# Kernel tuning notes

Measured on AMD Instinct MI355X. Metric: run time of the kernel, lower is better.

The kernel has to match this reference:

```python
import jax, jax.numpy as jnp
import numpy as np
import math

NUM_HEADS = 16
EMBED = 1024
B, S = 128, 512


def setup_inputs() -> dict:
    key = jax.random.key(0)
    ks = jax.random.split(key, 9)
    scale = 1.0 / math.sqrt(EMBED)
    return {
        "queries": jax.random.normal(ks[0], (B, S, EMBED), dtype=jnp.float32),
        "keys": jax.random.normal(ks[1], (B, S, EMBED), dtype=jnp.float32),
        "values": jax.random.normal(ks[2], (B, S, EMBED), dtype=jnp.float32),
        "Wq": jax.random.normal(ks[3], (EMBED, EMBED), dtype=jnp.float32) * scale,
        "bq": jax.random.normal(ks[4], (EMBED,), dtype=jnp.float32) * scale,
        "Wk": jax.random.normal(ks[5], (EMBED, EMBED), dtype=jnp.float32) * scale,
        "bk": jax.random.normal(ks[6], (EMBED,), dtype=jnp.float32) * scale,
        "Wv": jax.random.normal(ks[7], (EMBED, EMBED), dtype=jnp.float32) * scale,
        "bv": jax.random.normal(ks[8], (EMBED,), dtype=jnp.float32) * scale,
    }


def reference(queries, keys, values, Wq, bq, Wk, bk, Wv, bv):
    H = NUM_HEADS
    E = queries.shape[-1]
    d = E // H
    # torch nn.Linear: y = x @ W.T + b
    q = queries @ Wq.T + bq  # [B, S, E]
    k = keys @ Wk.T + bk
    v = values @ Wv.T + bv
    n_q = q.shape[1]
    n_k = k.shape[1]
    n_v = v.shape[1]
    # Faithful to the original: reshape with seq-len as the LEADING dim,
    # which reinterprets the (B, S, E) buffer as (S, B, H, d).
    q = q.reshape(n_q, -1, H, d)  # [S, B, H, d]
    k = k.reshape(n_k, -1, H, d)
    # attention over the second (batch-like) axis; scores: [S, H, B, B]
    scores = jnp.einsum('nqhd,nkhd->nhqk', q, k) / math.sqrt(d)
    attn = jax.nn.softmax(scores, axis=-1)
    v = v.reshape(n_v, -1, H, d)  # [S, B, H, d]
    out = jnp.einsum('nhql,nlhd->nqhd', attn, v)  # [S, B, H, d]
    n_a = out.shape[0]
    return out.reshape(-1, n_a, H * d)  # [B, S, E]
```

## Files before the change

kernel.cpp:

```cpp
#include <hip/hip_runtime.h>
#include <hip/hip_bf16.h>

typedef unsigned short u16;
typedef __attribute__((ext_vector_type(8))) short bf16x8;
typedef __attribute__((ext_vector_type(4))) float f32x4;
typedef __attribute__((ext_vector_type(4))) float vfloat4;
typedef __attribute__((ext_vector_type(4))) unsigned short ushort4v;
typedef __attribute__((ext_vector_type(8))) unsigned short ushort8v;

#define DEV __device__ __forceinline__
#define AS1 __attribute__((address_space(1)))
#define AS3 __attribute__((address_space(3)))

#define BARRIER()  __builtin_amdgcn_s_barrier()
#define LGKM0()    asm volatile("s_waitcnt lgkmcnt(0)" ::: "memory")
#define VMCNT0()   asm volatile("s_waitcnt vmcnt(0)" ::: "memory")
#define VMCNT4()   asm volatile("s_waitcnt vmcnt(4)" ::: "memory")
#define SCHED0()   __builtin_amdgcn_sched_barrier(0)

DEV u16 f2bf(float f) {
    union { float f; unsigned u; } v; v.f = f;
    unsigned r = v.u + 0x7FFFu + ((v.u >> 16) & 1u);
    return (u16)(r >> 16);
}

DEV void gload_lds16(const void* g, void* l) {
    __builtin_amdgcn_global_load_lds((const AS1 unsigned int*)g,
                                     (AS3 unsigned int*)l, 16, 0, 0);
}

static constexpr int KDIM = 1024;
static constexpr int NROW = 65536;

__global__ __launch_bounds__(256)
void cvt_f32_bf16(const float* __restrict__ src, u16* __restrict__ dst, unsigned n8)
{
    unsigned stride = gridDim.x * blockDim.x;
    for (unsigned i = blockIdx.x * blockDim.x + threadIdx.x; i < n8; i += stride) {
        size_t base = (size_t)i * 8;
        vfloat4 a = *(const vfloat4*)(src + base);
        vfloat4 b = *(const vfloat4*)(src + base + 4);
        ushort8v o;
#pragma unroll
        for (int j = 0; j < 4; ++j) { o[j] = f2bf(a[j]); o[j + 4] = f2bf(b[j]); }
        *(ushort8v*)(dst + base) = o;
    }
}

__global__ __launch_bounds__(512)
__attribute__((amdgpu_waves_per_eu(1, 2)))
void proj_gemm_8ph(const u16* __restrict__ X, const u16* __restrict__ W,
                   const float* __restrict__ bias, u16* __restrict__ Y)
{
    __shared__ __align__(16) u16 As[2][256 * 64];
    __shared__ __align__(16) u16 Bs[2][256 * 64];

    int bx = blockIdx.x;
    int wg = (bx & 7) * 128 + (bx >> 3);
    int bm = wg >> 2;
    int bn = wg & 3;

    int tid  = threadIdx.x;
    int lane = tid & 63;
    int wid  = tid >> 6;
    int wm   = wid >> 2;
    int wn   = wid & 3;
    int l15  = lane & 15;
    int l4   = lane >> 4;

    const u16* Xp = X + (size_t)bm * 256 * KDIM;
    const u16* Wp = W + (size_t)bn * 256 * KDIM;

    int srow_in = tid >> 3;
    int scol16  = (tid & 7) ^ (srow_in & 7);

    f32x4 acc[8][4] = {};

#define STAGE(lds, gbase, slot, h, kt)                                           \
    {                                                                            \
        const u16* src_ = (gbase) + (size_t)((h) * 128 + srow_in) * KDIM         \
                          + (kt) * 64 + scol16 * 8;                              \
        gload_lds16(src_, &lds[slot][((h) * 128 + wid * 8) * 64]);               \
        gload_lds16(src_ + (size_t)64 * KDIM,                                    \
                    &lds[slot][((h) * 128 + 64 + wid * 8) * 64]);                \
    }

#define READ_AF(slot, mh)                                                        \
    {                                                                            \
        _Pragma("unroll")                                                        \
        for (int mi = 0; mi < 4; ++mi) {                                         \
            int row = wm * 128 + (mh) * 64 + mi * 16 + l15;                      \
            unsigned o0 = (unsigned)(row * 128 + l4 * 16) ^ (unsigned)((row & 7) << 4); \
            af[mi][0] = *(const bf16x8*)((const char*)As[slot] + o0);            \
            af[mi][1] = *(const bf16x8*)((const char*)As[slot] + (o0 ^ 64u));    \
        }                                                                        \
    }

#define READ_BF(dst, slot, nh)                                                   \
    {                                                                            \
        _Pragma("unroll")                                                        \
        for (int ni = 0; ni < 2; ++ni) {                                         \
            int row = wn * 64 + (nh) * 32 + ni * 16 + l15;                       \
            unsigned o0 = (unsigned)(row * 128 + l4 * 16) ^ (unsigned)((row & 7) << 4); \
            dst[ni][0] = *(const bf16x8*)((const char*)Bs[slot] + o0);           \
            dst[ni][1] = *(const bf16x8*)((const char*)Bs[slot] + (o0 ^ 64u));   \
        }                                                                        \
    }

#define MFMA_Q(mlo, bb, nlo)                                                     \
    __builtin_amdgcn_s_setprio(1);                                               \
    _Pragma("unroll")                                                            \
    for (int kk = 0; kk < 2; ++kk) {                                             \
        _Pragma("unroll")                                                        \
        for (int mi = 0; mi < 4; ++mi) {                                         \
            _Pragma("unroll")                                                    \
            for (int ni = 0; ni < 2; ++ni)                                       \
                acc[(mlo) + mi][(nlo) + ni] = __builtin_amdgcn_mfma_f32_16x16x32_bf16( \
                    af[mi][kk], bb[ni][kk], acc[(mlo) + mi][(nlo) + ni], 0, 0, 0); \
        }                                                                        \
    }                                                                            \
    __builtin_amdgcn_s_setprio(0);

    STAGE(As, Xp, 0, 0, 0);
    STAGE(As, Xp, 0, 1, 0);
    STAGE(Bs, Wp, 0, 0, 0);
    STAGE(Bs, Wp, 0, 1, 0);
    STAGE(As, Xp, 1, 0, 1);
    STAGE(As, Xp, 1, 1, 1);
    STAGE(Bs, Wp, 1, 0, 1);
    STAGE(Bs, Wp, 1, 1, 1);
    VMCNT0();
    BARRIER();

    for (int it = 0; it < 8; ++it) {
        int c12 = 2 * it + 1;
        int c36 = (2 * it + 2 < 16) ? 2 * it + 2 : 15;
        int c78 = (2 * it + 3 < 16) ? 2 * it + 3 : 15;
        bf16x8 af[4][2], b0[2][2], b1[2][2];

        READ_AF(0, 0); READ_BF(b0, 0, 0);
        STAGE(As, Xp, 1, 0, c12);
        BARRIER(); LGKM0(); SCHED0();
        MFMA_Q(0, b0, 0);
        BARRIER();

        READ_BF(b1, 0, 1);
        STAGE(As, Xp, 1, 1, c12);
        BARRIER(); LGKM0(); SCHED0();
        MFMA_Q(0, b1, 2);
        BARRIER();

        READ_AF(0, 1);
        STAGE(Bs, Wp, 0, 0, c36);
        BARRIER(); LGKM0(); SCHED0();
        MFMA_Q(4, b1, 2);
        BARRIER();

        STAGE(Bs, Wp, 0, 1, c36);
        VMCNT4(); BARRIER(); SCHED0();
        MFMA_Q(4, b0, 0);
        BARRIER();

        READ_AF(1, 0); READ_BF(b0, 1, 0);
        STAGE(As, Xp, 0, 0, c36);
        BARRIER(); LGKM0(); SCHED0();
        MFMA_Q(0, b0, 0);
        BARRIER();

        READ_BF(b1, 1, 1);
        STAGE(As, Xp, 0, 1, c36);
        BARRIER(); LGKM0(); SCHED0();
        MFMA_Q(0, b1, 2);
        BARRIER();

        READ_AF(1, 1);
        STAGE(Bs, Wp, 1, 0, c78);
        BARRIER(); LGKM0(); SCHED0();
        MFMA_Q(4, b1, 2);
        BARRIER();

        STAGE(Bs, Wp, 1, 1, c78);
        VMCNT4(); BARRIER(); SCHED0();
        MFMA_Q(4, b0, 0);
        BARRIER();
    }
    VMCNT0();
    BARRIER();

    u16* Cs = &As[0][0];
#pragma unroll
    for (int p = 0; p < 2; ++p) {
        if (wm == p) {
#pragma unroll
            for (int ni = 0; ni < 4; ++ni) {
                float bv = bias[bn * 256 + wn * 64 + ni * 16 + l15];
#pragma unroll
                for (int mi = 0; mi < 8; ++mi) {
                    int lr0 = mi * 16 + l4 * 4;
                    int c   = wn * 64 + ni * 16 + l15;
#pragma unroll
                    for (int r = 0; r < 4; ++r)
                        Cs[(lr0 + r) * 256 + c] = f2bf(acc[mi][ni][r] + bv);
                }
            }
        }
        __syncthreads();
#pragma unroll
        for (int i = 0; i < 8; ++i) {
            int idx = tid + i * 512;
            int row = idx >> 5;
            int c16 = idx & 31;
            ushort8v v = *(const ushort8v*)&Cs[row * 256 + c16 * 8];
            *(ushort8v*)&Y[(size_t)(bm * 256 + p * 128 + row) * KDIM
                           + bn * 256 + c16 * 8] = v;
        }
        __syncthreads();
    }
#undef STAGE
#undef READ_AF
#undef READ_BF
#undef MFMA_Q
}

__global__ __launch_bounds__(256)
void proj_gemm(const float* __restrict__ X, const float* __restrict__ W,
               const float* __restrict__ bias, u16* __restrict__ Y)
{
    __shared__ u16 As[128 * 64];
    __shared__ u16 Bs[128 * 64];

    int bx = blockIdx.x;
    int wg = (bx & 7) * 512 + (bx >> 3);
    int bm = wg >> 3;
    int bn = wg & 7;

    int tid  = threadIdx.x;
    int lane = tid & 63;
    int wid  = tid >> 6;
    int wrow = (wid >> 1) * 64;
    int wcol = (wid & 1) * 64;
    int l15 = lane & 15;
    int l4  = lane >> 4;

    int srow = tid >> 4;
    int scol = (tid & 15) * 4;

    const float* Xp = X + (size_t)bm * 128 * KDIM;
    const float* Wp = W + (size_t)bn * 128 * KDIM;

    f32x4 acc[4][4] = {};

    for (int k0 = 0; k0 < KDIM; k0 += 64) {
        __syncthreads();
#pragma unroll
        for (int r = 0; r < 8; ++r) {
            int row = r * 16 + srow;
            vfloat4 a = *(const vfloat4*)(Xp + (size_t)row * KDIM + k0 + scol);
            vfloat4 b = *(const vfloat4*)(Wp + (size_t)row * KDIM + k0 + scol);
            ushort4v ap, bp;
#pragma unroll
            for (int j = 0; j < 4; ++j) { ap[j] = f2bf(a[j]); bp[j] = f2bf(b[j]); }
            unsigned off = (unsigned)(row * 128 + scol * 2) ^ (unsigned)((row & 7) << 4);
            *(ushort4v*)((char*)As + off) = ap;
            *(ushort4v*)((char*)Bs + off) = bp;
        }
        __syncthreads();
#pragma unroll
        for (int kk = 0; kk < 2; ++kk) {
            bf16x8 af[4], bfr[4];
#pragma unroll
            for (int mi = 0; mi < 4; ++mi) {
                int row = wrow + mi * 16 + l15;
                unsigned off = (unsigned)(row * 128 + kk * 64 + l4 * 16) ^ (unsigned)((row & 7) << 4);
                af[mi] = *(const bf16x8*)((char*)As + off);
            }
#pragma unroll
            for (int ni = 0; ni < 4; ++ni) {
                int row = wcol + ni * 16 + l15;
                unsigned off = (unsigned)(row * 128 + kk * 64 + l4 * 16) ^ (unsigned)((row & 7) << 4);
                bfr[ni] = *(const bf16x8*)((char*)Bs + off);
            }
#pragma unroll
            for (int mi = 0; mi < 4; ++mi)
#pragma unroll
                for (int ni = 0; ni < 4; ++ni)
                    acc[mi][ni] = __builtin_amdgcn_mfma_f32_16x16x32_bf16(
                        af[mi], bfr[ni], acc[mi][ni], 0, 0, 0);
        }
    }

#pragma unroll
    for (int ni = 0; ni < 4; ++ni) {
        int col = bn * 128 + wcol + ni * 16 + l15;
        float bv = bias[col];
#pragma unroll
        for (int mi = 0; mi < 4; ++mi) {
            int row0 = bm * 128 + wrow + mi * 16 + l4 * 4;
#pragma unroll
            for (int r = 0; r < 4; ++r)
                Y[(size_t)(row0 + r) * KDIM + col] = f2bf(acc[mi][ni][r] + bv);
        }
    }
}

__global__ __launch_bounds__(256)
void attn_kernel(const u16* __restrict__ Qg, const u16* __restrict__ Kg,
                 const u16* __restrict__ Vg, float* __restrict__ Out)
{
    __shared__ u16 Qs[128 * 64];
    __shared__ u16 KVs[64 * 136];
    __shared__ u16 Ps[128 * 136];

    int g = blockIdx.x >> 4;
    int h = blockIdx.x & 15;

    int tid  = threadIdx.x;
    int lane = tid & 63;
    int wid  = tid >> 6;
    int l15 = lane & 15, l4 = lane >> 4;
    int qbase = wid * 32;

    size_t rowbase = (size_t)g * 128 * 1024 + (size_t)h * 64;

    {
        int r  = tid >> 1;
        int c0 = (tid & 1) * 32;
        const u16* qsrc = Qg + rowbase + (size_t)r * 1024 + c0;
        const u16* ksrc = Kg + rowbase + (size_t)r * 1024 + c0;
#pragma unroll
        for (int i = 0; i < 4; ++i) {
            ushort8v qv = *(const ushort8v*)(qsrc + i * 8);
            ushort8v kv = *(const ushort8v*)(ksrc + i * 8);
            unsigned off = (unsigned)(r * 128 + (c0 + i * 8) * 2) ^ (unsigned)((r & 7) << 4);
            *(ushort8v*)((char*)Qs + off) = qv;
            *(ushort8v*)((char*)KVs + off) = kv;
        }
    }
    __syncthreads();

    f32x4 st[8][2] = {};
#pragma unroll
    for (int kk = 0; kk < 2; ++kk) {
        bf16x8 kf[8];
#pragma unroll
        for (int mi = 0; mi < 8; ++mi) {
            int row = mi * 16 + l15;
            unsigned off = (unsigned)(row * 128 + kk * 64 + l4 * 16) ^ (unsigned)((row & 7) << 4);
            kf[mi] = *(const bf16x8*)((char*)KVs + off);
        }
#pragma unroll
        for (int qi = 0; qi < 2; ++qi) {
            int row = qbase + qi * 16 + l15;
            unsigned off = (unsigned)(row * 128 + kk * 64 + l4 * 16) ^ (unsigned)((row & 7) << 4);
            bf16x8 qf = *(const bf16x8*)((char*)Qs + off);
#pragma unroll
            for (int mi = 0; mi < 8; ++mi)
                st[mi][qi] = __builtin_amdgcn_mfma_f32_16x16x32_bf16(kf[mi], qf, st[mi][qi], 0, 0, 0);
        }
    }
    __syncthreads();

    {
        int r  = tid >> 1;
        int c0 = (tid & 1) * 32;
        const u16* vsrc = Vg + rowbase + (size_t)r * 1024 + c0;
#pragma unroll
        for (int i = 0; i < 4; ++i) {
            ushort8v vv = *(const ushort8v*)(vsrc + i * 8);
#pragma unroll
            for (int e = 0; e < 8; ++e)
                KVs[(c0 + i * 8 + e) * 136 + r] = vv[e];
        }
    }

    const float cexp = 0.125f * 1.44269504088896f;
#pragma unroll
    for (int qi = 0; qi < 2; ++qi) {
        float m = -3.0e38f;
#pragma unroll
        for (int mi = 0; mi < 8; ++mi)
#pragma unroll
            for (int r = 0; r < 4; ++r) m = fmaxf(m, st[mi][qi][r]);
        m = fmaxf(m, __shfl_xor(m, 16));
        m = fmaxf(m, __shfl_xor(m, 32));
        float s = 0.f;
#pragma unroll
        for (int mi = 0; mi < 8; ++mi)
#pragma unroll
            for (int r = 0; r < 4; ++r) {
                float p = exp2f((st[mi][qi][r] - m) * cexp);
                st[mi][qi][r] = p;
                s += p;
            }
        s += __shfl_xor(s, 16);
        s += __shfl_xor(s, 32);
        float inv = 1.0f / s;
        int q = qbase + qi * 16 + l15;
#pragma unroll
        for (int mi = 0; mi < 8; ++mi) {
            ushort4v pp;
#pragma unroll
            for (int r = 0; r < 4; ++r) pp[r] = f2bf(st[mi][qi][r] * inv);
            *(ushort4v*)((char*)Ps + (unsigned)(q * 272 + mi * 32 + l4 * 8)) = pp;
        }
    }
    __syncthreads();

    f32x4 o[2][4] = {};
#pragma unroll
    for (int kk = 0; kk < 4; ++kk) {
        bf16x8 pa[2];
#pragma unroll
        for (int mf = 0; mf < 2; ++mf) {
            int q = qbase + mf * 16 + l15;
            pa[mf] = *(const bf16x8*)((char*)Ps + (unsigned)(q * 272 + kk * 64 + l4 * 16));
        }
#pragma unroll
        for (int nf = 0; nf < 4; ++nf) {
            int d = nf * 16 + l15;
            bf16x8 vb = *(const bf16x8*)((char*)KVs + (unsigned)(d * 272 + kk * 64 + l4 * 16));
#pragma unroll
            for (int mf = 0; mf < 2; ++mf)
                o[mf][nf] = __builtin_amdgcn_mfma_f32_16x16x32_bf16(pa[mf], vb, o[mf][nf], 0, 0, 0);
        }
    }

#pragma unroll
    for (int mf = 0; mf < 2; ++mf)
#pragma unroll
        for (int nf = 0; nf < 4; ++nf) {
            int d  = nf * 16 + l15;
            int q0 = qbase + mf * 16 + l4 * 4;
#pragma unroll
            for (int r = 0; r < 4; ++r)
                Out[(size_t)(g * 128 + q0 + r) * 1024 + h * 64 + d] = o[mf][nf][r];
        }
}

extern "C" void kernel_launch(void* const* d_in, const int* in_sizes, int n_in,
                              void* d_out, int out_size, void* d_ws, size_t ws_size,
                              hipStream_t stream)
{
    const float* Xq = (const float*)d_in[0];
    const float* Xk = (const float*)d_in[1];
    const float* Xv = (const float*)d_in[2];
    const float* Wq = (const float*)d_in[3];
    const float* bq = (const float*)d_in[4];
    const float* Wk = (const float*)d_in[5];
    const float* bk = (const float*)d_in[6];
    const float* Wv = (const float*)d_in[7];
    const float* bv = (const float*)d_in[8];

    const size_t NE = (size_t)NROW * KDIM;
    const size_t WE = (size_t)KDIM * KDIM;

    u16* Qw = (u16*)d_ws;
    u16* Kw = Qw + NE;
    u16* Vw = Kw + NE;

    size_t need = NE * 2 * 3 + NE * 2 + WE * 2 * 3;

    if (ws_size >= need) {
        u16* Xb  = Vw + NE;
        u16* Wb0 = Xb + NE;
        u16* Wb1 = Wb0 + WE;
        u16* Wb2 = Wb1 + WE;

        cvt_f32_bf16<<<dim3(512),  dim3(256), 0, stream>>>(Wq, Wb0, (unsigned)(WE / 8));
        cvt_f32_bf16<<<dim3(512),  dim3(256), 0, stream>>>(Wk, Wb1, (unsigned)(WE / 8));
        cvt_f32_bf16<<<dim3(512),  dim3(256), 0, stream>>>(Wv, Wb2, (unsigned)(WE / 8));

        cvt_f32_bf16<<<dim3(2048), dim3(256), 0, stream>>>(Xq, Xb, (unsigned)(NE / 8));
        proj_gemm_8ph<<<dim3(1024), dim3(512), 0, stream>>>(Xb, Wb0, bq, Qw);
        cvt_f32_bf16<<<dim3(2048), dim3(256), 0, stream>>>(Xk, Xb, (unsigned)(NE / 8));
        proj_gemm_8ph<<<dim3(1024), dim3(512), 0, stream>>>(Xb, Wb1, bk, Kw);
        cvt_f32_bf16<<<dim3(2048), dim3(256), 0, stream>>>(Xv, Xb, (unsigned)(NE / 8));
        proj_gemm_8ph<<<dim3(1024), dim3(512), 0, stream>>>(Xb, Wb2, bv, Vw);
    } else {
        proj_gemm<<<dim3(4096), dim3(256), 0, stream>>>(Xq, Wq, bq, Qw);
        proj_gemm<<<dim3(4096), dim3(256), 0, stream>>>(Xk, Wk, bk, Kw);
        proj_gemm<<<dim3(4096), dim3(256), 0, stream>>>(Xv, Wv, bv, Vw);
    }

    attn_kernel<<<dim3(512 * 16), dim3(256), 0, stream>>>(Qw, Kw, Vw, (float*)d_out);
}
```

Measured before the change: 846.8 us.

## Merge GEMM main-loop phases into four and XOR-swizzle epilogue staging buffer

Restructures the main GEMM loop from eight barrier-separated phases into four, issuing both B-fragment reads and both staging loads per phase and running two MFMA quads per phase. This halves the number of barriers and waits per iteration. It also applies an XOR swizzle to the shared-memory epilogue buffer to reduce LDS bank conflicts on both the scattered writes and the vectorized reads. The risks are higher register pressure and less fine-grained interleaving of global loads with compute.

```diff
diff --git a/kernel.cpp b/kernel.cpp
--- a/kernel.cpp
+++ b/kernel.cpp
@@ -138,50 +138,28 @@
         int c78 = (2 * it + 3 < 16) ? 2 * it + 3 : 15;
         bf16x8 af[4][2], b0[2][2], b1[2][2];
 
-        READ_AF(0, 0); READ_BF(b0, 0, 0);
-        STAGE(As, Xp, 1, 0, c12);
+        READ_AF(0, 0); READ_BF(b0, 0, 0); READ_BF(b1, 0, 1);
+        STAGE(As, Xp, 1, 0, c12); STAGE(As, Xp, 1, 1, c12);
         BARRIER(); LGKM0(); SCHED0();
-        MFMA_Q(0, b0, 0);
+        MFMA_Q(0, b0, 0); MFMA_Q(0, b1, 2);
         BARRIER();
 
-        READ_BF(b1, 0, 1);
-        STAGE(As, Xp, 1, 1, c12);
+        READ_AF(0, 1);
+        STAGE(Bs, Wp, 0, 0, c36); STAGE(Bs, Wp, 0, 1, c36);
+        VMCNT4(); BARRIER(); LGKM0(); SCHED0();
+        MFMA_Q(4, b0, 0); MFMA_Q(4, b1, 2);
+        BARRIER();
+
+        READ_AF(1, 0); READ_BF(b0, 1, 0); READ_BF(b1, 1, 1);
+        STAGE(As, Xp, 0, 0, c36); STAGE(As, Xp, 0, 1, c36);
         BARRIER(); LGKM0(); SCHED0();
-        MFMA_Q(0, b1, 2);
+        MFMA_Q(0, b0, 0); MFMA_Q(0, b1, 2);
         BARRIER();
 
-        READ_AF(0, 1);
-        STAGE(Bs, Wp, 0, 0, c36);
-        BARRIER(); LGKM0(); SCHED0();
-        MFMA_Q(4, b1, 2);
-        BARRIER();
-
-        STAGE(Bs, Wp, 0, 1, c36);
-        VMCNT4(); BARRIER(); SCHED0();
-        MFMA_Q(4, b0, 0);
-        BARRIER();
-
-        READ_AF(1, 0); READ_BF(b0, 1, 0);
-        STAGE(As, Xp, 0, 0, c36);
-        BARRIER(); LGKM0(); SCHED0();
-        MFMA_Q(0, b0, 0);
-        BARRIER();
-
-        READ_BF(b1, 1, 1);
-        STAGE(As, Xp, 0, 1, c36);
-        BARRIER(); LGKM0(); SCHED0();
-        MFMA_Q(0, b1, 2);
-        BARRIER();
-
         READ_AF(1, 1);
-        STAGE(Bs, Wp, 1, 0, c78);
-        BARRIER(); LGKM0(); SCHED0();
-        MFMA_Q(4, b1, 2);
-        BARRIER();
-
-        STAGE(Bs, Wp, 1, 1, c78);
-        VMCNT4(); BARRIER(); SCHED0();
-        MFMA_Q(4, b0, 0);
+        STAGE(Bs, Wp, 1, 0, c78); STAGE(Bs, Wp, 1, 1, c78);
+        VMCNT4(); BARRIER(); LGKM0(); SCHED0();
+        MFMA_Q(4, b0, 0); MFMA_Q(4, b1, 2);
         BARRIER();
     }
     VMCNT0();
@@ -196,11 +174,13 @@
                 float bv = bias[bn * 256 + wn * 64 + ni * 16 + l15];
 #pragma unroll
                 for (int mi = 0; mi < 8; ++mi) {
-                    int lr0 = mi * 16 + l4 * 4;
-                    int c   = wn * 64 + ni * 16 + l15;
-#pragma unroll
-                    for (int r = 0; r < 4; ++r)
-                        Cs[(lr0 + r) * 256 + c] = f2bf(acc[mi][ni][r] + bv);
+                    int c2 = (wn * 64 + ni * 16 + l15) * 2;
+#pragma unroll
+                    for (int r = 0; r < 4; ++r) {
+                        int row = mi * 16 + l4 * 4 + r;
+                        unsigned off = (unsigned)(row * 512 + c2) ^ (unsigned)((row & 7) << 4);
+                        *(u16*)((char*)Cs + off) = f2bf(acc[mi][ni][r] + bv);
+                    }
                 }
             }
         }
@@ -210,7 +190,8 @@
             int idx = tid + i * 512;
             int row = idx >> 5;
             int c16 = idx & 31;
-            ushort8v v = *(const ushort8v*)&Cs[row * 256 + c16 * 8];
+            unsigned off = (unsigned)(row * 512 + c16 * 16) ^ (unsigned)((row & 7) << 4);
+            ushort8v v = *(const ushort8v*)((const char*)Cs + off);
             *(ushort8v*)&Y[(size_t)(bm * 256 + p * 128 + row) * KDIM
                            + bn * 256 + c16 * 8] = v;
         }
```

Result: no change. 850.2 us (+0.4%).

## Merge weight and input conversions into one launch and swizzle epilogue LDS

Applied to the files above, without the earlier changes.

Adds a combined conversion kernel that turns all three weight matrices and two input tensors to bf16 in a single launch, using a second input staging buffer when the workspace is large enough. This cuts the number of small kernel launches. The GEMM epilogue now XOR-swizzles its LDS staging addresses by row, to reduce bank conflicts when scattering accumulators and reading them back as 16-byte vectors. It needs more workspace and falls back to the old path if that space is not available.

```diff
diff --git a/kernel.cpp b/kernel.cpp
--- a/kernel.cpp
+++ b/kernel.cpp
@@ -24,26 +24,49 @@
     return (u16)(r >> 16);
 }
 
+static constexpr int KDIM = 1024;
+static constexpr int NROW = 65536;
+
 DEV void gload_lds16(const void* g, void* l) {
     __builtin_amdgcn_global_load_lds((const AS1 unsigned int*)g,
                                      (AS3 unsigned int*)l, 16, 0, 0);
 }
 
-static constexpr int KDIM = 1024;
-static constexpr int NROW = 65536;
+DEV void cvt8(const float* __restrict__ src, u16* __restrict__ dst, size_t j) {
+    size_t base = j * 8;
+    vfloat4 a = *(const vfloat4*)(src + base);
+    vfloat4 b = *(const vfloat4*)(src + base + 4);
+    ushort8v o;
+#pragma unroll
+    for (int e = 0; e < 4; ++e) { o[e] = f2bf(a[e]); o[e + 4] = f2bf(b[e]); }
+    *(ushort8v*)(dst + base) = o;
+}
 
 __global__ __launch_bounds__(256)
 void cvt_f32_bf16(const float* __restrict__ src, u16* __restrict__ dst, unsigned n8)
 {
     unsigned stride = gridDim.x * blockDim.x;
-    for (unsigned i = blockIdx.x * blockDim.x + threadIdx.x; i < n8; i += stride) {
-        size_t base = (size_t)i * 8;
-        vfloat4 a = *(const vfloat4*)(src + base);
-        vfloat4 b = *(const vfloat4*)(src + base + 4);
-        ushort8v o;
-#pragma unroll
-        for (int j = 0; j < 4; ++j) { o[j] = f2bf(a[j]); o[j + 4] = f2bf(b[j]); }
-        *(ushort8v*)(dst + base) = o;
+    for (unsigned i = blockIdx.x * blockDim.x + threadIdx.x; i < n8; i += stride)
+        cvt8(src, dst, i);
+}
+
+__global__ __launch_bounds__(256)
+void cvt5(const float* __restrict__ Wq, const float* __restrict__ Wk,
+          const float* __restrict__ Wv, const float* __restrict__ Xq,
+          const float* __restrict__ Xk,
+          u16* __restrict__ Wb0, u16* __restrict__ Wb1, u16* __restrict__ Wb2,
+          u16* __restrict__ Xb0, u16* __restrict__ Xb1)
+{
+    const unsigned nW = (unsigned)((size_t)KDIM * KDIM / 8);
+    const unsigned nX = (unsigned)((size_t)NROW * KDIM / 8);
+    const unsigned total = 3 * nW + 2 * nX;
+    unsigned stride = gridDim.x * blockDim.x;
+    for (unsigned i = blockIdx.x * blockDim.x + threadIdx.x; i < total; i += stride) {
+        if (i < nW)                 cvt8(Wq, Wb0, i);
+        else if (i < 2 * nW)        cvt8(Wk, Wb1, i - nW);
+        else if (i < 3 * nW)        cvt8(Wv, Wb2, i - 2 * nW);
+        else if (i < 3 * nW + nX)   cvt8(Xq, Xb0, i - 3 * nW);
+        else                        cvt8(Xk, Xb1, i - 3 * nW - nX);
     }
 }
 
@@ -196,11 +219,13 @@
                 float bv = bias[bn * 256 + wn * 64 + ni * 16 + l15];
 #pragma unroll
                 for (int mi = 0; mi < 8; ++mi) {
-                    int lr0 = mi * 16 + l4 * 4;
-                    int c   = wn * 64 + ni * 16 + l15;
-#pragma unroll
-                    for (int r = 0; r < 4; ++r)
-                        Cs[(lr0 + r) * 256 + c] = f2bf(acc[mi][ni][r] + bv);
+                    int c2 = (wn * 64 + ni * 16 + l15) * 2;
+#pragma unroll
+                    for (int r = 0; r < 4; ++r) {
+                        int row = mi * 16 + l4 * 4 + r;
+                        unsigned off = (unsigned)(row * 512 + c2) ^ (unsigned)((row & 7) << 4);
+                        *(u16*)((char*)Cs + off) = f2bf(acc[mi][ni][r] + bv);
+                    }
                 }
             }
         }
@@ -210,7 +235,8 @@
             int idx = tid + i * 512;
             int row = idx >> 5;
             int c16 = idx & 31;
-            ushort8v v = *(const ushort8v*)&Cs[row * 256 + c16 * 8];
+            unsigned off = (unsigned)(row * 512 + c16 * 16) ^ (unsigned)((row & 7) << 4);
+            ushort8v v = *(const ushort8v*)((const char*)Cs + off);
             *(ushort8v*)&Y[(size_t)(bm * 256 + p * 128 + row) * KDIM
                            + bn * 256 + c16 * 8] = v;
         }
@@ -458,9 +484,23 @@
     u16* Kw = Qw + NE;
     u16* Vw = Kw + NE;
 
-    size_t need = NE * 2 * 3 + NE * 2 + WE * 2 * 3;
-
-    if (ws_size >= need) {
+    size_t need2 = NE * 2 * 3 + NE * 2 * 2 + WE * 2 * 3;
+    size_t need1 = NE * 2 * 3 + NE * 2     + WE * 2 * 3;
+
+    if (ws_size >= need2) {
+        u16* Xb0 = Vw + NE;
+        u16* Xb1 = Xb0 + NE;
+        u16* Wb0 = Xb1 + NE;
+        u16* Wb1 = Wb0 + WE;
+        u16* Wb2 = Wb1 + WE;
+
+        cvt5<<<dim3(2048), dim3(256), 0, stream>>>(Wq, Wk, Wv, Xq, Xk,
+                                                   Wb0, Wb1, Wb2, Xb0, Xb1);
+        proj_gemm_8ph<<<dim3(1024), dim3(512), 0, stream>>>(Xb0, Wb0, bq, Qw);
+        cvt_f32_bf16<<<dim3(2048), dim3(256), 0, stream>>>(Xv, Xb0, (unsigned)(NE / 8));
+        proj_gemm_8ph<<<dim3(1024), dim3(512), 0, stream>>>(Xb1, Wb1, bk, Kw);
+        proj_gemm_8ph<<<dim3(1024), dim3(512), 0, stream>>>(Xb0, Wb2, bv, Vw);
+    } else if (ws_size >= need1) {
         u16* Xb  = Vw + NE;
         u16* Wb0 = Xb + NE;
         u16* Wb1 = Wb0 + WE;
```

Result: slower. 866.1 us (+2.3%).
